# Kernel tuning notes

Measured on AMD Instinct MI355X. Metric: run time of the kernel, lower is better.

The kernel has to match this reference:

```python
import jax, jax.numpy as jnp
import numpy as np

FP8_MAX = 448.0  # float8_e4m3fn max
NUM_HEADS = 16

def _fp8_quant_dequant(t):
    # per-(batch, head) symmetric scaling into fp8 e4m3 range, cast to fp8 and back
    amax = jnp.max(jnp.abs(t), axis=(-2, -1), keepdims=True)
    scale = FP8_MAX / jnp.maximum(amax, 1e-12)
    t8 = (t * scale).astype(jnp.float8_e4m3fn).astype(t.dtype)
    return t8 / scale

def setup_inputs() -> dict:
    key = jax.random.key(0)
    k1, k2, k3 = jax.random.split(key, 3)
    B, N, C = 2, 2048, 1024
    x = jax.random.normal(k1, (B, N, C), dtype=jnp.float32)
    w_qkv = jax.random.normal(k2, (C, 3 * C), dtype=jnp.float32) * (C ** -0.5)
    w_proj = jax.random.normal(k3, (C, C), dtype=jnp.float32) * (C ** -0.5)
    b_proj = jnp.zeros((C,), dtype=jnp.float32)
    return {"x": x, "w_qkv": w_qkv, "w_proj": w_proj, "b_proj": b_proj}

def reference(x, w_qkv, w_proj, b_proj):
    B, N, C = x.shape
    H = NUM_HEADS
    D = C // H
    scale = D ** -0.5
    qkv = (x @ w_qkv).reshape(B, N, 3, H, D).transpose(2, 0, 3, 1, 4)  # [3,B,H,N,D]
    q, k, v = qkv[0], qkv[1], qkv[2]
    # sage-style fp8 quantize/dequant of q and k fused into score computation
    q = _fp8_quant_dequant(q)
    k = _fp8_quant_dequant(k)
    scores = jnp.einsum('bhqd,bhkd->bhqk', q, k) * scale  # [B,H,N,N]
    causal = jnp.tril(jnp.ones((N, N), dtype=bool))
    scores = jnp.where(causal[None, None], scores, jnp.finfo(scores.dtype).min)
    attn = jax.nn.softmax(scores, axis=-1)
    out = jnp.einsum('bhqk,bhkd->bhqd', attn, v)  # [B,H,N,D]
    out = out.transpose(0, 2, 1, 3).reshape(B, N, C)
    return out @ w_proj + b_proj
```

## Files before the change

kernel.cpp:

```cpp
#include <hip/hip_runtime.h>

#define B_   2
#define N_   2048
#define C_   1024
#define H_   16
#define D_   64
#define BH_  (B_*H_)
#define NDH  (N_*D_)
#define M1   (B_*N_)

typedef __attribute__((ext_vector_type(4))) float    f32x4;
typedef __attribute__((ext_vector_type(8))) _Float16 f16x8;
typedef __attribute__((ext_vector_type(4))) _Float16 f16x4;

__global__ void k_cvt16(const float* __restrict__ in, _Float16* __restrict__ out, int n4) {
  int i = blockIdx.x * blockDim.x + threadIdx.x;
  if (i >= n4) return;
  float4 v = ((const float4*)in)[i];
  f16x4 o;
  o.x = (_Float16)v.x; o.y = (_Float16)v.y; o.z = (_Float16)v.z; o.w = (_Float16)v.w;
  ((f16x4*)out)[i] = o;
}

__global__ __launch_bounds__(256) void k_transmerge(const float* __restrict__ wq,
                                                    const float* __restrict__ wp,
                                                    _Float16* __restrict__ whT,
                                                    _Float16* __restrict__ wpT,
                                                    unsigned* __restrict__ amax_u) {
  if (blockIdx.x == 0 && threadIdx.x < 64) amax_u[threadIdx.x] = 0u;
  __shared__ _Float16 t[64][68];
  int idx = blockIdx.x;
  const float* in; _Float16* out; int Cc, cx, cy;
  if (idx < 768) { in = wq; out = whT; Cc = 3072; cx = idx % 48; cy = idx / 48; }
  else { idx -= 768; in = wp; out = wpT; Cc = 1024; cx = idx % 16; cy = idx / 16; }
  const int R = 1024;
  int c0 = cx * 64, r0 = cy * 64;
  int tid = threadIdx.x;
  int cq = tid & 15, rq = tid >> 4;
#pragma unroll
  for (int i = 0; i < 4; ++i) {
    int r = rq + i * 16;
    float4 v = *(const float4*)(in + (size_t)(r0 + r) * Cc + c0 + cq * 4);
    t[r][cq*4+0] = (_Float16)v.x;
    t[r][cq*4+1] = (_Float16)v.y;
    t[r][cq*4+2] = (_Float16)v.z;
    t[r][cq*4+3] = (_Float16)v.w;
  }
  __syncthreads();
#pragma unroll
  for (int i = 0; i < 4; ++i) {
    int c = rq + i * 16;
    f16x4 o;
    o.x = t[cq*4+0][c];
    o.y = t[cq*4+1][c];
    o.z = t[cq*4+2][c];
    o.w = t[cq*4+3][c];
    *(f16x4*)(out + (size_t)(c0 + c) * R + r0 + cq * 4) = o;
  }
}

__global__ __launch_bounds__(256) void k_gemm_qkv(const _Float16* __restrict__ A,
                                                  const _Float16* __restrict__ BT,
                                                  float* __restrict__ qf,
                                                  float* __restrict__ kf,
                                                  _Float16* __restrict__ vh,
                                                  unsigned* __restrict__ amax_u) {
  __shared__ __align__(16) _Float16 As[128 * 40];
  __shared__ __align__(16) _Float16 Bs[128 * 40];
  const int tid = threadIdx.x, lane = tid & 63, wave = tid >> 6;
  const int wm = wave >> 1, wn = wave & 1;
  const int mcol = lane & 15, quad = lane >> 4;
  const int m0 = blockIdx.x * 128, n0 = blockIdx.y * 128;
  f32x4 acc[4][4] = {};
  for (int k0 = 0; k0 < 1024; k0 += 32) {
#pragma unroll
    for (int r = 0; r < 2; ++r) {
      int chunk = tid + r * 256;
      int row = chunk >> 2, kc = chunk & 3;
      *(int4*)&As[row * 40 + kc * 8] = *(const int4*)(A  + (size_t)(m0 + row) * 1024 + k0 + kc * 8);
      *(int4*)&Bs[row * 40 + kc * 8] = *(const int4*)(BT + (size_t)(n0 + row) * 1024 + k0 + kc * 8);
    }
    __syncthreads();
    f16x8 af[4], bf[4];
#pragma unroll
    for (int tm = 0; tm < 4; ++tm)
      af[tm] = *(const f16x8*)&As[(wm * 64 + tm * 16 + mcol) * 40 + quad * 8];
#pragma unroll
    for (int tn = 0; tn < 4; ++tn)
      bf[tn] = *(const f16x8*)&Bs[(wn * 64 + tn * 16 + mcol) * 40 + quad * 8];
#pragma unroll
    for (int tm = 0; tm < 4; ++tm)
#pragma unroll
      for (int tn = 0; tn < 4; ++tn)
        acc[tm][tn] = __builtin_amdgcn_mfma_f32_16x16x32_f16(af[tm], bf[tn], acc[tm][tn], 0, 0, 0);
    __syncthreads();
  }
  const int sec = n0 >> 10;
  if (sec < 2) {
    float* dst = sec ? kf : qf;
    float mxv = 0.f;
#pragma unroll
    for (int tm = 0; tm < 4; ++tm)
#pragma unroll
      for (int tn = 0; tn < 4; ++tn)
#pragma unroll
        for (int reg = 0; reg < 4; ++reg) {
          int row = m0 + wm * 64 + tm * 16 + quad * 4 + reg;
          int col = n0 + wn * 64 + tn * 16 + mcol;
          int cc = col & 1023, h = cc >> 6, d = cc & 63;
          int b = row >> 11, n = row & 2047;
          float v = acc[tm][tn][reg];
          mxv = fmaxf(mxv, fabsf(v));
          dst[((size_t)(b * 16 + h) * 2048 + n) * 64 + d] = v;
        }
#pragma unroll
    for (int off = 32; off; off >>= 1) mxv = fmaxf(mxv, __shfl_xor(mxv, off));
    if (lane == 0) {
      int head = ((n0 & 1023) >> 6) + wn;
      int plane = (m0 >> 11) * 16 + head;
      atomicMax(&amax_u[sec * 32 + plane], __float_as_uint(mxv));
    }
  } else {
#pragma unroll
    for (int tm = 0; tm < 4; ++tm)
#pragma unroll
      for (int tn = 0; tn < 4; ++tn) {
        int rowb = m0 + wm * 64 + tm * 16 + quad * 4;
        int col = n0 + wn * 64 + tn * 16 + mcol;
        int cc = col & 1023, h = cc >> 6, d = cc & 63;
        int b = rowb >> 11, n = rowb & 2047;
        f16x4 o;
        o.x = (_Float16)acc[tm][tn][0];
        o.y = (_Float16)acc[tm][tn][1];
        o.z = (_Float16)acc[tm][tn][2];
        o.w = (_Float16)acc[tm][tn][3];
        *(f16x4*)&vh[(size_t)(b * 16 + h) * 131072 + (size_t)(n >> 5) * 2048 + d * 32 + (n & 31)] = o;
      }
  }
}

__global__ __launch_bounds__(256) void k_quant(const float* __restrict__ qf,
                                               const float* __restrict__ kf,
                                               const float* __restrict__ amax,
                                               char* __restrict__ q8,
                                               char* __restrict__ k8) {
  int blk = blockIdx.x;
  int which = blk >> 11;
  int idx = blk & 2047;
  int bh = idx >> 6, chunk = idx & 63;
  const float* src = (which ? kf : qf) + (size_t)bh * NDH + chunk * 2048;
  float s = 448.f / fmaxf(amax[which * 32 + bh], 1e-12f);
  int t = threadIdx.x;
  float4 a = ((const float4*)(src + t * 8))[0];
  float4 c = ((const float4*)(src + t * 8))[1];
  int lo = 0, hi = 0;
  lo = __builtin_amdgcn_cvt_pk_fp8_f32(a.x * s, a.y * s, lo, false);
  lo = __builtin_amdgcn_cvt_pk_fp8_f32(a.z * s, a.w * s, lo, true);
  hi = __builtin_amdgcn_cvt_pk_fp8_f32(c.x * s, c.y * s, hi, false);
  hi = __builtin_amdgcn_cvt_pk_fp8_f32(c.z * s, c.w * s, hi, true);
  int2 o; o.x = lo; o.y = hi;
  if (which == 0) {
    char* dst = q8 + (size_t)bh * NDH + chunk * 2048;
    *(int2*)(dst + t * 8) = o;
  } else {
    int kk = t >> 3, d0 = (t & 7) * 8;
    int e = (kk >> 2) & 1;
    int mc = (kk >> 3) * 4 + (kk & 3);
    int kb = d0 >> 5, dq = (d0 >> 3) & 3;
    char* dst = k8 + (size_t)bh * NDH + chunk * 2048 + (e * 2 + kb) * 512 + mc * 32 + dq * 8;
    *(int2*)dst = o;
  }
}

__global__ __launch_bounds__(256, 2) void k_flash(const char* __restrict__ q8,
                                                  const char* __restrict__ k8,
                                                  const _Float16* __restrict__ vh,
                                                  const float* __restrict__ amax,
                                                  _Float16* __restrict__ attn) {
  const int bh = blockIdx.x;
  const int wave = threadIdx.x >> 6, lane = threadIdx.x & 63;
  const int mcol = lane & 15, quad = lane >> 4;
  const int pr = blockIdx.y * 4 + wave;
  const int ga = pr, gb = 127 - pr;
  const int ta = (ga >> 3) + 1;

  float sq = 448.f / fmaxf(amax[bh], 1e-12f);
  float sk = 448.f / fmaxf(amax[32 + bh], 1e-12f);
  const float c2 = (1.f / (sq * sk)) * 0.125f * 1.44269504089f;

  const size_t pbase = (size_t)bh * NDH;
  const char* kbase = k8 + pbase + mcol * 32 + quad * 8;
  const _Float16* vbase = vh + pbase + mcol * 32 + quad * 8;
  const int qrowA = ga * 16 + mcol, qrowB = gb * 16 + mcol;
  long aqA0, aqA1, aqB0, aqB1;
  { const char* qp = q8 + pbase + (size_t)qrowA * 64;
    aqA0 = *(const long*)(qp + quad * 8); aqA1 = *(const long*)(qp + 32 + quad * 8); }
  { const char* qp = q8 + pbase + (size_t)qrowB * 64;
    aqB0 = *(const long*)(qp + quad * 8); aqB1 = *(const long*)(qp + 32 + quad * 8); }

  f32x4 O[4] = {};
  float m_i = -3e38f, l_i = 0.f;
  const int b = bh >> 4, h = bh & 15;
  const int kq = quad * 8;

  long kc[16], kn[16];
  {
    const char* kp = kbase;
#pragma unroll
    for (int i = 0; i < 16; ++i) kc[i] = *(const long*)(kp + i * 512);
  }

  auto body = [&](int t, long (&cur)[16], long (&nxt)[16]) {
    const bool inB = t >= ta;
    const int n0 = (inB ? t - ta : t) * 128;
    const long aq0 = inB ? aqB0 : aqA0;
    const long aq1 = inB ? aqB1 : aqA1;
    const int qrow = inB ? qrowB : qrowA;
    const bool last = inB ? (t == 16) : (t == ta - 1);

    f32x4 s[4][2];
#pragma unroll
    for (int p = 0; p < 4; ++p)
#pragma unroll
      for (int e = 0; e < 2; ++e) {
        f32x4 z = {};
        z = __builtin_amdgcn_mfma_f32_16x16x32_fp8_fp8(cur[p * 4 + e * 2 + 0], aq0, z, 0, 0, 0);
        z = __builtin_amdgcn_mfma_f32_16x16x32_fp8_fp8(cur[p * 4 + e * 2 + 1], aq1, z, 0, 0, 0);
        s[p][e] = z;
      }
    f16x8 va[4][4];
    {
      const _Float16* vp = vbase + (size_t)(n0 >> 5) * 2048;
#pragma unroll
      for (int p = 0; p < 4; ++p)
#pragma unroll
        for (int dt = 0; dt < 4; ++dt)
          va[dt][p] = *(const f16x8*)(vp + p * 2048 + dt * 512);
    }
    if (t < 16) {
      const int t2 = t + 1;
      const int n02 = ((t2 >= ta) ? t2 - ta : t2) * 128;
      const char* kp = kbase + (size_t)(n02 >> 5) * 2048;
#pragma unroll
      for (int i = 0; i < 16; ++i) nxt[i] = *(const long*)(kp + i * 512);
    }
    if (last) {
#pragma unroll
      for (int p = 0; p < 4; ++p)
#pragma unroll
        for (int e = 0; e < 2; ++e)
#pragma unroll
          for (int r = 0; r < 4; ++r) {
            int key = n0 + p * 32 + kq + e * 4 + r;
            float v = s[p][e][r] * c2;
            s[p][e][r] = (key <= qrow) ? v : -3e38f;
          }
    } else {
#pragma unroll
      for (int p = 0; p < 4; ++p)
#pragma unroll
        for (int e = 0; e < 2; ++e)
#pragma unroll
          for (int r = 0; r < 4; ++r)
            s[p][e][r] = s[p][e][r] * c2;
    }
    float fm[8];
#pragma unroll
    for (int p = 0; p < 4; ++p)
#pragma unroll
      for (int e = 0; e < 2; ++e) {
        f32x4 v = s[p][e];
        fm[p * 2 + e] = fmaxf(fmaxf(v[0], v[1]), fmaxf(v[2], v[3]));
      }
    float mx = fmaxf(fmaxf(fmaxf(fm[0], fm[1]), fmaxf(fm[2], fm[3])),
                     fmaxf(fmaxf(fm[4], fm[5]), fmaxf(fm[6], fm[7])));
    mx = fmaxf(mx, m_i);
    mx = fmaxf(mx, __shfl_xor(mx, 16));
    mx = fmaxf(mx, __shfl_xor(mx, 32));
    float alpha = exp2f(m_i - mx);
    m_i = mx;
    float fs[8];
#pragma unroll
    for (int p = 0; p < 4; ++p)
#pragma unroll
      for (int e = 0; e < 2; ++e) {
        float p0 = exp2f(s[p][e][0] - mx);
        float p1 = exp2f(s[p][e][1] - mx);
        float p2 = exp2f(s[p][e][2] - mx);
        float p3 = exp2f(s[p][e][3] - mx);
        s[p][e][0] = p0; s[p][e][1] = p1; s[p][e][2] = p2; s[p][e][3] = p3;
        fs[p * 2 + e] = (p0 + p1) + (p2 + p3);
      }
    float sum = ((fs[0] + fs[1]) + (fs[2] + fs[3])) + ((fs[4] + fs[5]) + (fs[6] + fs[7]));
    sum += __shfl_xor(sum, 16);
    sum += __shfl_xor(sum, 32);
    l_i = l_i * alpha + sum;
#pragma unroll
    for (int dt = 0; dt < 4; ++dt)
#pragma unroll
      for (int r = 0; r < 4; ++r)
        O[dt][r] *= alpha;
#pragma unroll
    for (int p = 0; p < 4; ++p) {
      f16x8 pb;
      pb[0] = (_Float16)s[p][0][0]; pb[1] = (_Float16)s[p][0][1];
      pb[2] = (_Float16)s[p][0][2]; pb[3] = (_Float16)s[p][0][3];
      pb[4] = (_Float16)s[p][1][0]; pb[5] = (_Float16)s[p][1][1];
      pb[6] = (_Float16)s[p][1][2]; pb[7] = (_Float16)s[p][1][3];
#pragma unroll
      for (int dt = 0; dt < 4; ++dt)
        O[dt] = __builtin_amdgcn_mfma_f32_16x16x32_f16(va[dt][p], pb, O[dt], 0, 0, 0);
    }
    if (last) {
      float rl = 1.f / l_i;
      _Float16* op = attn + ((size_t)b * 2048 + qrow) * 1024 + h * 64;
#pragma unroll
      for (int dt = 0; dt < 4; ++dt) {
        f16x4 o;
        o.x = (_Float16)(O[dt][0] * rl);
        o.y = (_Float16)(O[dt][1] * rl);
        o.z = (_Float16)(O[dt][2] * rl);
        o.w = (_Float16)(O[dt][3] * rl);
        *(f16x4*)(op + dt * 16 + quad * 4) = o;
        O[dt] = (f32x4){0.f, 0.f, 0.f, 0.f};
      }
      m_i = -3e38f; l_i = 0.f;
    }
  };

#pragma unroll 1
  for (int t = 0; t < 17; t += 2) {
    body(t, kc, kn);
    if (t + 1 < 17) body(t + 1, kn, kc);
  }
}

__global__ __launch_bounds__(256) void k_gemm_out(const _Float16* __restrict__ A,
                                                  const _Float16* __restrict__ BT,
                                                  const float* __restrict__ bias,
                                                  float* __restrict__ out) {
  __shared__ __align__(16) _Float16 As[128 * 40];
  __shared__ __align__(16) _Float16 Bs[128 * 40];
  const int tid = threadIdx.x, lane = tid & 63, wave = tid >> 6;
  const int wm = wave >> 1, wn = wave & 1;
  const int mcol = lane & 15, quad = lane >> 4;
  const int m0 = blockIdx.x * 128, n0 = blockIdx.y * 128;
  f32x4 acc[4][4] = {};
  for (int k0 = 0; k0 < 1024; k0 += 32) {
#pragma unroll
    for (int r = 0; r < 2; ++r) {
      int chunk = tid + r * 256;
      int row = chunk >> 2, kc = chunk & 3;
      *(int4*)&As[row * 40 + kc * 8] = *(const int4*)(A  + (size_t)(m0 + row) * 1024 + k0 + kc * 8);
      *(int4*)&Bs[row * 40 + kc * 8] = *(const int4*)(BT + (size_t)(n0 + row) * 1024 + k0 + kc * 8);
    }
    __syncthreads();
    f16x8 af[4], bf[4];
#pragma unroll
    for (int tm = 0; tm < 4; ++tm)
      af[tm] = *(const f16x8*)&As[(wm * 64 + tm * 16 + mcol) * 40 + quad * 8];
#pragma unroll
    for (int tn = 0; tn < 4; ++tn)
      bf[tn] = *(const f16x8*)&Bs[(wn * 64 + tn * 16 + mcol) * 40 + quad * 8];
#pragma unroll
    for (int tm = 0; tm < 4; ++tm)
#pragma unroll
      for (int tn = 0; tn < 4; ++tn)
        acc[tm][tn] = __builtin_amdgcn_mfma_f32_16x16x32_f16(af[tm], bf[tn], acc[tm][tn], 0, 0, 0);
    __syncthreads();
  }
#pragma unroll
  for (int tm = 0; tm < 4; ++tm)
#pragma unroll
    for (int tn = 0; tn < 4; ++tn)
#pragma unroll
      for (int reg = 0; reg < 4; ++reg) {
        int row = m0 + wm * 64 + tm * 16 + quad * 4 + reg;
        int col = n0 + wn * 64 + tn * 16 + mcol;
        out[(size_t)row * 1024 + col] = acc[tm][tn][reg] + bias[col];
      }
}

extern "C" void kernel_launch(void* const* d_in, const int* in_sizes, int n_in,
                              void* d_out, int out_size, void* d_ws, size_t ws_size,
                              hipStream_t stream) {
  const float* x      = (const float*)d_in[0];
  const float* w_qkv  = (const float*)d_in[1];
  const float* w_proj = (const float*)d_in[2];
  const float* b_proj = (const float*)d_in[3];
  float* out = (float*)d_out;

  char* ws = (char*)d_ws;
  _Float16* xh   = (_Float16*)ws; ws += (size_t)M1 * C_ * 2;
  _Float16* whT  = (_Float16*)ws; ws += (size_t)3 * C_ * C_ * 2;
  _Float16* wpT  = (_Float16*)ws; ws += (size_t)C_ * C_ * 2;
  float*    qf   = (float*)ws;    ws += (size_t)BH_ * NDH * 4;
  float*    kf   = (float*)ws;    ws += (size_t)BH_ * NDH * 4;
  _Float16* vh   = (_Float16*)ws; ws += (size_t)BH_ * NDH * 2;
  char*     q8   = (char*)ws;     ws += (size_t)BH_ * NDH;
  char*     k8   = (char*)ws;     ws += (size_t)BH_ * NDH;
  _Float16* attn = (_Float16*)ws; ws += (size_t)M1 * C_ * 2;
  float*    amx  = (float*)ws;    ws += 256;

  k_cvt16<<<(M1 * C_ / 4 + 255) / 256, 256, 0, stream>>>(x, xh, M1 * C_ / 4);
  k_transmerge<<<1024, 256, 0, stream>>>(w_qkv, w_proj, whT, wpT, (unsigned*)amx);
  k_gemm_qkv<<<dim3(M1 / 128, 3 * C_ / 128), 256, 0, stream>>>(xh, whT, qf, kf, vh, (unsigned*)amx);
  k_quant<<<4096, 256, 0, stream>>>(qf, kf, amx, q8, k8);
  k_flash<<<dim3(32, 16), 256, 0, stream>>>(q8, k8, vh, amx, attn);
  k_gemm_out<<<dim3(M1 / 128, C_ / 128), 256, 0, stream>>>(attn, wpT, b_proj, out);
}
```

Measured before the change: 225.1 us.

## Use direct global-to-LDS loads in GEMMs and store Q/K as fp16

GEMM tile loads now use global_load_lds to bypass registers, and the LDS padding is removed. The QKV GEMM writes Q and K as fp16 in a tiled transposed layout with vector stores instead of fp32 scattered stores. The quant kernel reads these fp16 values and transposes them back through shared memory. This halves intermediate traffic and removes uncoalesced stores, at the risk of LDS bank conflicts from the unpadded stride and an extra fp16 rounding before fp8 quantization.

```diff
diff --git a/kernel.cpp b/kernel.cpp
--- a/kernel.cpp
+++ b/kernel.cpp
@@ -12,6 +12,10 @@
 typedef __attribute__((ext_vector_type(4))) float    f32x4;
 typedef __attribute__((ext_vector_type(8))) _Float16 f16x8;
 typedef __attribute__((ext_vector_type(4))) _Float16 f16x4;
+
+#define GLOAD_LDS(gp, lp) \
+  __builtin_amdgcn_global_load_lds((const __attribute__((address_space(1))) void*)(gp), \
+                                   (__attribute__((address_space(3))) void*)(lp), 16, 0, 0)
 
 __global__ void k_cvt16(const float* __restrict__ in, _Float16* __restrict__ out, int n4) {
   int i = blockIdx.x * blockDim.x + threadIdx.x;
@@ -61,12 +65,12 @@
 
 __global__ __launch_bounds__(256) void k_gemm_qkv(const _Float16* __restrict__ A,
                                                   const _Float16* __restrict__ BT,
-                                                  float* __restrict__ qf,
-                                                  float* __restrict__ kf,
+                                                  _Float16* __restrict__ qh,
+                                                  _Float16* __restrict__ kh,
                                                   _Float16* __restrict__ vh,
                                                   unsigned* __restrict__ amax_u) {
-  __shared__ __align__(16) _Float16 As[128 * 40];
-  __shared__ __align__(16) _Float16 Bs[128 * 40];
+  __shared__ __align__(16) _Float16 As[128 * 32];
+  __shared__ __align__(16) _Float16 Bs[128 * 32];
   const int tid = threadIdx.x, lane = tid & 63, wave = tid >> 6;
   const int wm = wave >> 1, wn = wave & 1;
   const int mcol = lane & 15, quad = lane >> 4;
@@ -75,19 +79,19 @@
   for (int k0 = 0; k0 < 1024; k0 += 32) {
 #pragma unroll
     for (int r = 0; r < 2; ++r) {
-      int chunk = tid + r * 256;
-      int row = chunk >> 2, kc = chunk & 3;
-      *(int4*)&As[row * 40 + kc * 8] = *(const int4*)(A  + (size_t)(m0 + row) * 1024 + k0 + kc * 8);
-      *(int4*)&Bs[row * 40 + kc * 8] = *(const int4*)(BT + (size_t)(n0 + row) * 1024 + k0 + kc * 8);
+      int c = tid + r * 256;
+      int row = c >> 2, kc = c & 3;
+      GLOAD_LDS(A  + (size_t)(m0 + row) * 1024 + k0 + kc * 8, &As[c * 8]);
+      GLOAD_LDS(BT + (size_t)(n0 + row) * 1024 + k0 + kc * 8, &Bs[c * 8]);
     }
     __syncthreads();
     f16x8 af[4], bf[4];
 #pragma unroll
     for (int tm = 0; tm < 4; ++tm)
-      af[tm] = *(const f16x8*)&As[(wm * 64 + tm * 16 + mcol) * 40 + quad * 8];
+      af[tm] = *(const f16x8*)&As[(wm * 64 + tm * 16 + mcol) * 32 + quad * 8];
 #pragma unroll
     for (int tn = 0; tn < 4; ++tn)
-      bf[tn] = *(const f16x8*)&Bs[(wn * 64 + tn * 16 + mcol) * 40 + quad * 8];
+      bf[tn] = *(const f16x8*)&Bs[(wn * 64 + tn * 16 + mcol) * 32 + quad * 8];
 #pragma unroll
     for (int tm = 0; tm < 4; ++tm)
 #pragma unroll
@@ -97,22 +101,24 @@
   }
   const int sec = n0 >> 10;
   if (sec < 2) {
-    float* dst = sec ? kf : qf;
+    _Float16* dst = sec ? kh : qh;
     float mxv = 0.f;
 #pragma unroll
     for (int tm = 0; tm < 4; ++tm)
 #pragma unroll
-      for (int tn = 0; tn < 4; ++tn)
-#pragma unroll
-        for (int reg = 0; reg < 4; ++reg) {
-          int row = m0 + wm * 64 + tm * 16 + quad * 4 + reg;
-          int col = n0 + wn * 64 + tn * 16 + mcol;
-          int cc = col & 1023, h = cc >> 6, d = cc & 63;
-          int b = row >> 11, n = row & 2047;
-          float v = acc[tm][tn][reg];
-          mxv = fmaxf(mxv, fabsf(v));
-          dst[((size_t)(b * 16 + h) * 2048 + n) * 64 + d] = v;
-        }
+      for (int tn = 0; tn < 4; ++tn) {
+        int rowb = m0 + wm * 64 + tm * 16 + quad * 4;
+        int col = n0 + wn * 64 + tn * 16 + mcol;
+        int cc = col & 1023, h = cc >> 6, d = cc & 63;
+        int b = rowb >> 11, n = rowb & 2047;
+        f32x4 a = acc[tm][tn];
+        mxv = fmaxf(mxv, fmaxf(fmaxf(fabsf(a[0]), fabsf(a[1])),
+                               fmaxf(fabsf(a[2]), fabsf(a[3]))));
+        f16x4 o;
+        o.x = (_Float16)a[0]; o.y = (_Float16)a[1];
+        o.z = (_Float16)a[2]; o.w = (_Float16)a[3];
+        *(f16x4*)&dst[(size_t)(b * 16 + h) * 131072 + (size_t)(n >> 5) * 2048 + d * 32 + (n & 31)] = o;
+      }
 #pragma unroll
     for (int off = 32; off; off >>= 1) mxv = fmaxf(mxv, __shfl_xor(mxv, off));
     if (lane == 0) {
@@ -139,33 +145,41 @@
   }
 }
 
-__global__ __launch_bounds__(256) void k_quant(const float* __restrict__ qf,
-                                               const float* __restrict__ kf,
+__global__ __launch_bounds__(256) void k_quant(const _Float16* __restrict__ qh,
+                                               const _Float16* __restrict__ kh,
                                                const float* __restrict__ amax,
                                                char* __restrict__ q8,
                                                char* __restrict__ k8) {
+  __shared__ ushort T[32][72];
   int blk = blockIdx.x;
   int which = blk >> 11;
   int idx = blk & 2047;
   int bh = idx >> 6, chunk = idx & 63;
-  const float* src = (which ? kf : qf) + (size_t)bh * NDH + chunk * 2048;
+  const _Float16* src = (which ? kh : qh) + (size_t)bh * NDH + chunk * 2048;
   float s = 448.f / fmaxf(amax[which * 32 + bh], 1e-12f);
   int t = threadIdx.x;
-  float4 a = ((const float4*)(src + t * 8))[0];
-  float4 c = ((const float4*)(src + t * 8))[1];
+  f16x8 v = *(const f16x8*)(src + t * 8);
+  int d = t >> 2, kk0 = (t & 3) * 8;
+#pragma unroll
+  for (int j = 0; j < 8; ++j) T[kk0 + j][d] = ((const ushort*)&v)[j];
+  __syncthreads();
+  int r = t >> 3, d0 = (t & 7) * 8;
+  f16x8 row = *(const f16x8*)&T[r][d0];
+  float f[8];
+#pragma unroll
+  for (int j = 0; j < 8; ++j) f[j] = (float)((const _Float16*)&row)[j] * s;
   int lo = 0, hi = 0;
-  lo = __builtin_amdgcn_cvt_pk_fp8_f32(a.x * s, a.y * s, lo, false);
-  lo = __builtin_amdgcn_cvt_pk_fp8_f32(a.z * s, a.w * s, lo, true);
-  hi = __builtin_amdgcn_cvt_pk_fp8_f32(c.x * s, c.y * s, hi, false);
-  hi = __builtin_amdgcn_cvt_pk_fp8_f32(c.z * s, c.w * s, hi, true);
+  lo = __builtin_amdgcn_cvt_pk_fp8_f32(f[0], f[1], lo, false);
+  lo = __builtin_amdgcn_cvt_pk_fp8_f32(f[2], f[3], lo, true);
+  hi = __builtin_amdgcn_cvt_pk_fp8_f32(f[4], f[5], hi, false);
+  hi = __builtin_amdgcn_cvt_pk_fp8_f32(f[6], f[7], hi, true);
   int2 o; o.x = lo; o.y = hi;
   if (which == 0) {
-    char* dst = q8 + (size_t)bh * NDH + chunk * 2048;
-    *(int2*)(dst + t * 8) = o;
+    char* dst = q8 + (size_t)bh * NDH + (size_t)(chunk * 32 + r) * 64 + d0;
+    *(int2*)dst = o;
   } else {
-    int kk = t >> 3, d0 = (t & 7) * 8;
-    int e = (kk >> 2) & 1;
-    int mc = (kk >> 3) * 4 + (kk & 3);
+    int e = (r >> 2) & 1;
+    int mc = (r >> 3) * 4 + (r & 3);
     int kb = d0 >> 5, dq = (d0 >> 3) & 3;
     char* dst = k8 + (size_t)bh * NDH + chunk * 2048 + (e * 2 + kb) * 512 + mc * 32 + dq * 8;
     *(int2*)dst = o;
@@ -339,8 +353,8 @@
                                                   const _Float16* __restrict__ BT,
                                                   const float* __restrict__ bias,
                                                   float* __restrict__ out) {
-  __shared__ __align__(16) _Float16 As[128 * 40];
-  __shared__ __align__(16) _Float16 Bs[128 * 40];
+  __shared__ __align__(16) _Float16 As[128 * 32];
+  __shared__ __align__(16) _Float16 Bs[128 * 32];
   const int tid = threadIdx.x, lane = tid & 63, wave = tid >> 6;
   const int wm = wave >> 1, wn = wave & 1;
   const int mcol = lane & 15, quad = lane >> 4;
@@ -349,19 +363,19 @@
   for (int k0 = 0; k0 < 1024; k0 += 32) {
 #pragma unroll
     for (int r = 0; r < 2; ++r) {
-      int chunk = tid + r * 256;
-      int row = chunk >> 2, kc = chunk & 3;
-      *(int4*)&As[row * 40 + kc * 8] = *(const int4*)(A  + (size_t)(m0 + row) * 1024 + k0 + kc * 8);
-      *(int4*)&Bs[row * 40 + kc * 8] = *(const int4*)(BT + (size_t)(n0 + row) * 1024 + k0 + kc * 8);
+      int c = tid + r * 256;
+      int row = c >> 2, kc = c & 3;
+      GLOAD_LDS(A  + (size_t)(m0 + row) * 1024 + k0 + kc * 8, &As[c * 8]);
+      GLOAD_LDS(BT + (size_t)(n0 + row) * 1024 + k0 + kc * 8, &Bs[c * 8]);
     }
     __syncthreads();
     f16x8 af[4], bf[4];
 #pragma unroll
     for (int tm = 0; tm < 4; ++tm)
-      af[tm] = *(const f16x8*)&As[(wm * 64 + tm * 16 + mcol) * 40 + quad * 8];
+      af[tm] = *(const f16x8*)&As[(wm * 64 + tm * 16 + mcol) * 32 + quad * 8];
 #pragma unroll
     for (int tn = 0; tn < 4; ++tn)
-      bf[tn] = *(const f16x8*)&Bs[(wn * 64 + tn * 16 + mcol) * 40 + quad * 8];
+      bf[tn] = *(const f16x8*)&Bs[(wn * 64 + tn * 16 + mcol) * 32 + quad * 8];
 #pragma unroll
     for (int tm = 0; tm < 4; ++tm)
 #pragma unroll
@@ -394,8 +408,8 @@
   _Float16* xh   = (_Float16*)ws; ws += (size_t)M1 * C_ * 2;
   _Float16* whT  = (_Float16*)ws; ws += (size_t)3 * C_ * C_ * 2;
   _Float16* wpT  = (_Float16*)ws; ws += (size_t)C_ * C_ * 2;
-  float*    qf   = (float*)ws;    ws += (size_t)BH_ * NDH * 4;
-  float*    kf   = (float*)ws;    ws += (size_t)BH_ * NDH * 4;
+  _Float16* qh   = (_Float16*)ws; ws += (size_t)BH_ * NDH * 2;
+  _Float16* kh   = (_Float16*)ws; ws += (size_t)BH_ * NDH * 2;
   _Float16* vh   = (_Float16*)ws; ws += (size_t)BH_ * NDH * 2;
   char*     q8   = (char*)ws;     ws += (size_t)BH_ * NDH;
   char*     k8   = (char*)ws;     ws += (size_t)BH_ * NDH;
@@ -404,8 +418,8 @@
 
   k_cvt16<<<(M1 * C_ / 4 + 255) / 256, 256, 0, stream>>>(x, xh, M1 * C_ / 4);
   k_transmerge<<<1024, 256, 0, stream>>>(w_qkv, w_proj, whT, wpT, (unsigned*)amx);
-  k_gemm_qkv<<<dim3(M1 / 128, 3 * C_ / 128), 256, 0, stream>>>(xh, whT, qf, kf, vh, (unsigned*)amx);
-  k_quant<<<4096, 256, 0, stream>>>(qf, kf, amx, q8, k8);
+  k_gemm_qkv<<<dim3(M1 / 128, 3 * C_ / 128), 256, 0, stream>>>(xh, whT, qh, kh, vh, (unsigned*)amx);
+  k_quant<<<4096, 256, 0, stream>>>(qh, kh, amx, q8, k8);
   k_flash<<<dim3(32, 16), 256, 0, stream>>>(q8, k8, vh, amx, attn);
   k_gemm_out<<<dim3(M1 / 128, C_ / 128), 256, 0, stream>>>(attn, wpT, b_proj, out);
 }
```

After: 215.4 us. 1.05x faster.
